# Kernel optimization log

Measured on AMD Instinct MI355X. Metric: run time of the kernel, lower is better.

Reference implementation:

```python
import jax, jax.numpy as jnp
import numpy as np

N = 100000
E = 1600000
IN_C = 128
HID = 256
K_EIG = 64
OUT_C = 16


def setup_inputs() -> dict:
    key = jax.random.key(0)
    ks = jax.random.split(key, 8)
    x = jax.random.normal(ks[0], (N, IN_C), dtype=jnp.float32)
    edge_index = jax.random.randint(ks[1], (2, E), 0, N)
    MLP_W = jax.random.normal(ks[2], (K_EIG, N), dtype=jnp.float32) * 0.02
    MLP_b = jax.random.normal(ks[3], (K_EIG,), dtype=jnp.float32) * 0.02
    mlpx_W = jax.random.normal(ks[4], (HID, IN_C), dtype=jnp.float32) * 0.05
    mlpx_b = jax.random.normal(ks[5], (HID,), dtype=jnp.float32) * 0.02
    fin_W = jax.random.normal(ks[6], (OUT_C, HID + K_EIG), dtype=jnp.float32) * 0.05
    fin_b = jax.random.normal(ks[7], (OUT_C,), dtype=jnp.float32) * 0.02
    return {"x": x, "edge_index": edge_index, "MLP_W": MLP_W, "MLP_b": MLP_b,
            "mlpx_W": mlpx_W, "mlpx_b": mlpx_b, "fin_W": fin_W, "fin_b": fin_b}


def _spmm(row, col, feats, n):
    # adj is COO with coords (col[e], row[e]) and value 1 -> out[col] += feats[row]
    return jax.ops.segment_sum(feats[row], col, num_segments=n)


def _pump(xA, row, col, n):
    # MinCut-style pump: soft assignment, normalized-cut loss + orthogonality loss
    S = jax.nn.softmax(xA, axis=-1)                      # [N, K]
    AS = _spmm(row, col, S, n)                            # A @ S, [N, K]
    cut = jnp.sum(S * AS)                                 # tr(S^T A S)
    deg = jax.ops.segment_sum(jnp.ones(col.shape, S.dtype), col, num_segments=n)
    deg_term = jnp.sum(deg[:, None] * S * S)              # tr(S^T D S)
    pump_loss = -(cut / deg_term)
    SS = S.T @ S                                          # [K, K]
    k = S.shape[1]
    ortho_loss = jnp.linalg.norm(SS / jnp.linalg.norm(SS)
                                 - jnp.eye(k, dtype=S.dtype) / jnp.sqrt(jnp.asarray(k, S.dtype)))
    return S, pump_loss, ortho_loss


def reference(x, edge_index, MLP_W, MLP_b, mlpx_W, mlpx_b, fin_W, fin_b):
    row, col = edge_index[0], edge_index[1]
    n = x.shape[0]
    # xA = adj @ MLP.weight.T + bias   (irregular gather/scatter over edges)
    xA = _spmm(row, col, MLP_W.T, n) + MLP_b              # [N, K]
    xX = x @ mlpx_W.T + mlpx_b                            # [N, HID]
    xA, pump_loss, ortho_loss = _pump(xA, row, col, n)
    z = jnp.concatenate([xX, xA], axis=1)                 # [N, HID+K]
    # dropout omitted (eval mode)
    z = jax.nn.log_softmax(z @ fin_W.T + fin_b, axis=-1)  # [N, OUT]
    return (z, pump_loss + ortho_loss)
```

## Files before the change

### kernel.cpp

```cpp
#include <hip/hip_runtime.h>
#include <math.h>

#define N_NODES 100000
#define N_EDGES 1600000
#define IN_C    128
#define HID     256
#define KEIG    64
#define OUT_C   16

#define NPB      256
#define NBUCKET  ((N_NODES + NPB - 1) / NPB)
#define EDGE_TILE 4096
#define NTILE    ((N_EDGES + EDGE_TILE - 1) / EDGE_TILE)
#define CAP      8960

#define TRANS_BLOCKS   ((N_NODES + 63) / 64)
#define GATHER_BLOCKS  2048
#define CUT_BLOCKS     2048
#define SSP_BLOCKS     512
#define OUTG_BLOCKS    384
#define TAIL_BLOCKS    (128 * 23)

typedef __attribute__((ext_vector_type(8))) short short8;
typedef __attribute__((ext_vector_type(4))) float f32x4;

__device__ __forceinline__ float wave_sum(float v) {
#pragma unroll
    for (int m = 32; m; m >>= 1) v += __shfl_xor(v, m, 64);
    return v;
}
__device__ __forceinline__ float wave_max(float v) {
#pragma unroll
    for (int m = 32; m; m >>= 1) v = fmaxf(v, __shfl_xor(v, m, 64));
    return v;
}
__device__ __forceinline__ float bf2f(unsigned int u) {
    return __uint_as_float((u & 0xffffu) << 16);
}
__device__ __forceinline__ unsigned short f2bf(float f) {
    unsigned int u = __float_as_uint(f);
    u += 0x7fff + ((u >> 16) & 1);
    return (unsigned short)(u >> 16);
}
__device__ __forceinline__ float fp8tof(int b) {
    return __builtin_amdgcn_cvt_f32_fp8(b, 0);
}
__device__ __forceinline__ unsigned char f2fp8(float f) {
    int p = __builtin_amdgcn_cvt_pk_fp8_f32(f, f, 0, false);
    return (unsigned char)(p & 0xff);
}

#define FMA4(P, s, W) \
    P.x = fmaf(s, W.x, P.x); P.y = fmaf(s, W.y, P.y); \
    P.z = fmaf(s, W.z, P.z); P.w = fmaf(s, W.w, P.w);

#define GATHER16(TBL, DST) do {                                               \
    int r0 = csr_row[ps + j + 0],  r1 = csr_row[ps + j + 1];                  \
    int r2 = csr_row[ps + j + 2],  r3 = csr_row[ps + j + 3];                  \
    int r4 = csr_row[ps + j + 4],  r5 = csr_row[ps + j + 5];                  \
    int r6 = csr_row[ps + j + 6],  r7 = csr_row[ps + j + 7];                  \
    int r8 = csr_row[ps + j + 8],  r9 = csr_row[ps + j + 9];                  \
    int rA = csr_row[ps + j + 10], rB = csr_row[ps + j + 11];                 \
    int rC = csr_row[ps + j + 12], rD = csr_row[ps + j + 13];                 \
    int rE = csr_row[ps + j + 14], rF = csr_row[ps + j + 15];                 \
    int b0 = TBL[(unsigned)r0 * 64u + lane], b1 = TBL[(unsigned)r1 * 64u + lane]; \
    int b2 = TBL[(unsigned)r2 * 64u + lane], b3 = TBL[(unsigned)r3 * 64u + lane]; \
    int b4 = TBL[(unsigned)r4 * 64u + lane], b5 = TBL[(unsigned)r5 * 64u + lane]; \
    int b6 = TBL[(unsigned)r6 * 64u + lane], b7 = TBL[(unsigned)r7 * 64u + lane]; \
    int b8 = TBL[(unsigned)r8 * 64u + lane], b9 = TBL[(unsigned)r9 * 64u + lane]; \
    int bA = TBL[(unsigned)rA * 64u + lane], bB = TBL[(unsigned)rB * 64u + lane]; \
    int bC = TBL[(unsigned)rC * 64u + lane], bD = TBL[(unsigned)rD * 64u + lane]; \
    int bE = TBL[(unsigned)rE * 64u + lane], bF = TBL[(unsigned)rF * 64u + lane]; \
    DST += (((fp8tof(b0) + fp8tof(b1)) + (fp8tof(b2) + fp8tof(b3)))           \
          + ((fp8tof(b4) + fp8tof(b5)) + (fp8tof(b6) + fp8tof(b7))))          \
         + (((fp8tof(b8) + fp8tof(b9)) + (fp8tof(bA) + fp8tof(bB)))           \
          + ((fp8tof(bC) + fp8tof(bD)) + (fp8tof(bE) + fp8tof(bF))));         \
} while (0)

__global__ void prep_weff(const float* __restrict__ mlpxW, const float* __restrict__ mlpxb,
                          const float* __restrict__ finW, const float* __restrict__ finb,
                          float* __restrict__ Weff, float* __restrict__ beff,
                          int* __restrict__ bcnt, unsigned char* __restrict__ WT8,
                          unsigned char* __restrict__ S8, int* __restrict__ gpad) {
    int t = blockIdx.x * blockDim.x + threadIdx.x;
    const int NW = (IN_C + KEIG) * OUT_C;
    if (t < NW) {
        int k = t >> 4, o = t & 15;
        float acc;
        if (k < IN_C) {
            acc = 0.f;
            for (int c = 0; c < HID; ++c)
                acc += mlpxW[c * IN_C + k] * finW[o * (HID + KEIG) + c];
        } else {
            acc = finW[o * (HID + KEIG) + HID + (k - IN_C)];
        }
        Weff[k * OUT_C + o] = acc;
    }
    int tb = t - NW;
    if (tb >= 0 && tb < OUT_C) {
        float acc = finb[tb];
        for (int c = 0; c < HID; ++c) acc += mlpxb[c] * finW[tb * (HID + KEIG) + c];
        beff[tb] = acc;
    }
    int tz = t - (NW + OUT_C);
    if (tz >= 0 && tz <= NBUCKET) bcnt[tz] = 0;
    int tp = t - (NW + OUT_C + NBUCKET + 1);
    if (tp >= 0 && tp < 16) {
        ((int*)(WT8 + (size_t)N_NODES * 64))[tp] = 0;
        ((int*)(S8 + (size_t)N_NODES * 64))[tp] = 0;
        if (tp == 0) *gpad = 0;
    }
}

__global__ __launch_bounds__(256) void fused_prep(const float* __restrict__ W,
                                                  unsigned char* __restrict__ WT8,
                                                  const int* __restrict__ ei,
                                                  int* __restrict__ bcnt) {
    __shared__ __align__(16) char sm[64 * 65 * 4];
    int t = threadIdx.x;
    if (blockIdx.x < TRANS_BLOCKS) {
        float (*tile)[65] = (float (*)[65])sm;
        int n0 = blockIdx.x * 64;
        int tn = t & 63, tq = t >> 6;
#pragma unroll
        for (int kk = 0; kk < 16; ++kk) {
            int k = tq * 16 + kk;
            int n = n0 + tn;
            tile[k][tn] = (n < N_NODES) ? W[(long long)k * N_NODES + n] : 0.f;
        }
        __syncthreads();
        int tk = t & 63;
#pragma unroll
        for (int ii = 0; ii < 16; ++ii) {
            int n = n0 + tq * 16 + ii;
            if (n < N_NODES) WT8[(unsigned)n * 64u + tk] = f2fp8(tile[tk][tq * 16 + ii] * 32.f);
        }
    } else {
        int* h = (int*)sm;
        for (int i = t; i < NBUCKET; i += 256) h[i] = 0;
        __syncthreads();
        int tile_i = blockIdx.x - TRANS_BLOCKS;
        int e0 = tile_i * EDGE_TILE;
        int e1 = min(e0 + EDGE_TILE, N_EDGES);
        for (int e = e0 + t; e < e1; e += 256)
            atomicAdd(&h[ei[N_EDGES + e] >> 8], 1);
        __syncthreads();
        for (int i = t; i < NBUCKET; i += 256)
            if (h[i]) atomicAdd(&bcnt[i], h[i]);
    }
}

__global__ void bucket_scan(const int* __restrict__ bcnt, int* __restrict__ bbase,
                            int* __restrict__ bcur) {
    __shared__ int sh[512];
    int t = threadIdx.x;
    int v = (t < NBUCKET) ? bcnt[t] : 0;
    sh[t] = v;
    __syncthreads();
    for (int d = 1; d < 512; d <<= 1) {
        int u = (t >= d) ? sh[t - d] : 0;
        __syncthreads();
        sh[t] += u;
        __syncthreads();
    }
    if (t < NBUCKET) { bbase[t] = sh[t] - v; bcur[t] = sh[t] - v; }
    if (t == 0) bbase[NBUCKET] = N_EDGES;
}

__global__ void bucket_scatter(const int* __restrict__ ei, int* __restrict__ bcur,
                               int* __restrict__ ebuf) {
    __shared__ int h[NBUCKET];
    __shared__ int gb[NBUCKET];
    __shared__ int lpre[NBUCKET];
    __shared__ int psum[256];
    __shared__ int stage[EDGE_TILE];
    __shared__ short bkt[EDGE_TILE];
    int t = threadIdx.x;
    for (int i = t; i < NBUCKET; i += 256) h[i] = 0;
    __syncthreads();
    int e0 = blockIdx.x * EDGE_TILE;
    int e1 = min(e0 + EDGE_TILE, N_EDGES);
    int nt = e1 - e0;
    for (int e = e0 + t; e < e1; e += 256)
        atomicAdd(&h[ei[N_EDGES + e] >> 8], 1);
    __syncthreads();
    int a0 = (2 * t < NBUCKET) ? h[2 * t] : 0;
    int a1 = (2 * t + 1 < NBUCKET) ? h[2 * t + 1] : 0;
    psum[t] = a0 + a1;
    __syncthreads();
    for (int d = 1; d < 256; d <<= 1) {
        int u = (t >= d) ? psum[t - d] : 0;
        __syncthreads();
        psum[t] += u;
        __syncthreads();
    }
    int base = (t == 0) ? 0 : psum[t - 1];
    if (2 * t < NBUCKET) lpre[2 * t] = base;
    if (2 * t + 1 < NBUCKET) lpre[2 * t + 1] = base + a0;
    __syncthreads();
    for (int i = t; i < NBUCKET; i += 256) {
        int c = h[i];
        gb[i] = c ? atomicAdd(&bcur[i], c) : 0;
        h[i] = lpre[i];
    }
    __syncthreads();
    for (int e = e0 + t; e < e1; e += 256) {
        int r = ei[e];
        int c = ei[N_EDGES + e];
        int b = c >> 8;
        int slot = atomicAdd(&h[b], 1);
        stage[slot] = r | ((c & 255) << 17);
        bkt[slot] = (short)b;
    }
    __syncthreads();
    for (int s = t; s < nt; s += 256) {
        int b = bkt[s];
        ebuf[gb[b] + s - lpre[b]] = stage[s];
    }
}

__global__ void csr_build(const int* __restrict__ ebuf, const int* __restrict__ bbase,
                          int* __restrict__ offsets, int* __restrict__ pstart,
                          int* __restrict__ csr_row, int* __restrict__ gpad) {
    __shared__ int hist[NPB];
    __shared__ int sh[NPB];
    __shared__ int curs[NPB];
    __shared__ int staged[CAP];
    __shared__ int pbase_sh;
    int b = blockIdx.x;
    int t = threadIdx.x;
    int s0 = bbase[b], s1 = bbase[b + 1];
    hist[t] = 0;
    __syncthreads();
    for (int i = s0 + t; i < s1; i += 256)
        atomicAdd(&hist[ebuf[i] >> 17], 1);
    __syncthreads();
    int v = hist[t];
    int pv = (v + 15) & ~15;
    sh[t] = pv;
    __syncthreads();
    for (int d = 1; d < 256; d <<= 1) {
        int u = (t >= d) ? sh[t - d] : 0;
        __syncthreads();
        sh[t] += u;
        __syncthreads();
    }
    int pexcl = sh[t] - pv;
    int pt = sh[255];
    if (t == 0) pbase_sh = atomicAdd(gpad, pt);
    __syncthreads();
    int pbase = pbase_sh;
    int node = b * NPB + t;
    if (node < N_NODES) { offsets[node] = v; pstart[node] = pbase + pexcl; }
    curs[t] = pexcl;
    __syncthreads();
    if (pt <= CAP) {
        for (int i = t; i < pt; i += 256) staged[i] = N_NODES;
        __syncthreads();
        for (int i = s0 + t; i < s1; i += 256) {
            int pk = ebuf[i];
            int pos = atomicAdd(&curs[pk >> 17], 1);
            staged[pos] = pk & 0x1FFFF;
        }
        __syncthreads();
        for (int i = t; i < pt; i += 256) csr_row[pbase + i] = staged[i];
    } else {
        for (int i = t; i < pt; i += 256) csr_row[pbase + i] = N_NODES;
        __syncthreads();
        for (int i = s0 + t; i < s1; i += 256) {
            int pk = ebuf[i];
            int pos = atomicAdd(&curs[pk >> 17], 1);
            csr_row[pbase + pos] = pk & 0x1FFFF;
        }
    }
}

__global__ void gather_softmax(const int* __restrict__ offsets, const int* __restrict__ pstart,
                               const int* __restrict__ csr_row,
                               const unsigned char* __restrict__ WT8,
                               const float* __restrict__ MLPb,
                               unsigned short* __restrict__ Sb,
                               unsigned char* __restrict__ S8,
                               float* __restrict__ dtp) {
    int lane = threadIdx.x & 63;
    int wib = __builtin_amdgcn_readfirstlane(threadIdx.x >> 6);
    int gw = blockIdx.x * 4 + wib;
    int nw = gridDim.x * 4;
    float bias = MLPb[lane];
    float dacc = 0.f;
    for (int n = gw; n < N_NODES; n += nw) {
        int deg = __builtin_amdgcn_readfirstlane(offsets[n]);
        int ps  = __builtin_amdgcn_readfirstlane(pstart[n]);
        int plen = (deg + 15) & ~15;
        float acc = 0.f;
        for (int j = 0; j < plen; j += 16) GATHER16(WT8, acc);
        acc = bias + acc * 0.03125f;
        float m = wave_max(acc);
        float e = __expf(acc - m);
        float sm = wave_sum(e);
        float sv = e / sm;
        unsigned idx = (unsigned)n * 64u + lane;
        Sb[idx] = f2bf(sv);
        S8[idx] = f2fp8(sv * 64.f);
        dacc += (float)deg * sv * sv;
    }
    dacc = wave_sum(dacc);
    __shared__ float red[4];
    if (lane == 0) red[wib] = dacc;
    __syncthreads();
    if (threadIdx.x == 0) dtp[blockIdx.x] = red[0] + red[1] + red[2] + red[3];
}

__global__ __launch_bounds__(256) void fused_tail(
        const int* __restrict__ offsets, const int* __restrict__ pstart,
        const int* __restrict__ csr_row,
        const unsigned short* __restrict__ Sb, const unsigned char* __restrict__ S8,
        float* __restrict__ cutp, float* __restrict__ ssp,
        const float* __restrict__ x, const float* __restrict__ Weff,
        const float* __restrict__ beff, float* __restrict__ out) {
    __shared__ __align__(16) char sm[768 * 16 + 64];
    int t = threadIdx.x;
    int grp = blockIdx.x / 23;
    int r23 = blockIdx.x % 23;

    if (r23 < 16) {
        int bid = grp * 16 + r23;
        int lane = t & 63;
        int wib = __builtin_amdgcn_readfirstlane(t >> 6);
        int gw = bid * 4 + wib;
        int nw = CUT_BLOCKS * 4;
        float acc = 0.f;
        for (int n = gw; n < N_NODES; n += nw) {
            float sc = bf2f(Sb[(unsigned)n * 64u + lane]);
            int deg = __builtin_amdgcn_readfirstlane(offsets[n]);
            int ps  = __builtin_amdgcn_readfirstlane(pstart[n]);
            int plen = (deg + 15) & ~15;
            float g = 0.f;
            for (int j = 0; j < plen; j += 16) GATHER16(S8, g);
            acc += sc * g * 0.015625f;
        }
        acc = wave_sum(acc);
        float* red = (float*)sm;
        if (lane == 0) red[wib] = acc;
        __syncthreads();
        if (t == 0) cutp[bid] = red[0] + red[1] + red[2] + red[3];
    } else if (r23 < 20) {
        int bid2 = grp * 4 + (r23 - 16);
        unsigned short (*Sr)[66] = (unsigned short (*)[66])sm;
        int lane = t & 63;
        int w = t >> 6;
        int m = lane & 15;
        int quad = lane >> 4;
        int srow = t >> 3;
        int spart = t & 7;
        f32x4 a0 = {0.f,0.f,0.f,0.f}, a1 = {0.f,0.f,0.f,0.f};
        f32x4 a2 = {0.f,0.f,0.f,0.f}, a3 = {0.f,0.f,0.f,0.f};
        for (int base = bid2 * 32; base < N_NODES; base += SSP_BLOCKS * 32) {
            const uint4* g = (const uint4*)(Sb + (long long)(base + srow) * 64 + spart * 8);
            uint4 d = *g;
            __syncthreads();
            unsigned int* rowp = (unsigned int*)&Sr[srow][0];
            rowp[spart * 4 + 0] = d.x;
            rowp[spart * 4 + 1] = d.y;
            rowp[spart * 4 + 2] = d.z;
            rowp[spart * 4 + 3] = d.w;
            __syncthreads();
            short8 f0, f1, f2, f3;
#pragma unroll
            for (int j = 0; j < 8; ++j) {
                int k = quad * 8 + j;
                f0[j] = (short)Sr[k][m];
                f1[j] = (short)Sr[k][16 + m];
                f2[j] = (short)Sr[k][32 + m];
                f3[j] = (short)Sr[k][48 + m];
            }
            short8 fa = (w == 0) ? f0 : (w == 1) ? f1 : (w == 2) ? f2 : f3;
            a0 = __builtin_amdgcn_mfma_f32_16x16x32_bf16(fa, f0, a0, 0, 0, 0);
            a1 = __builtin_amdgcn_mfma_f32_16x16x32_bf16(fa, f1, a1, 0, 0, 0);
            a2 = __builtin_amdgcn_mfma_f32_16x16x32_bf16(fa, f2, a2, 0, 0, 0);
            a3 = __builtin_amdgcn_mfma_f32_16x16x32_bf16(fa, f3, a3, 0, 0, 0);
        }
        float* dst = ssp + (size_t)bid2 * 4096;
#pragma unroll
        for (int r = 0; r < 4; ++r) {
            int row = w * 16 + quad * 4 + r;
            dst[row * 64 +  0 + m] = a0[r];
            dst[row * 64 + 16 + m] = a1[r];
            dst[row * 64 + 32 + m] = a2[r];
            dst[row * 64 + 48 + m] = a3[r];
        }
    } else {
        int obid = grp * 3 + (r23 - 20);
        float4* Wsh = (float4*)sm;
        float* bsh = (float*)(sm + 768 * 16);
        const float4* W4 = (const float4*)Weff;
        for (int i = t; i < 768; i += 256) Wsh[i] = W4[i];
        if (t < 16) bsh[t] = beff[t];
        __syncthreads();
        for (int r = obid * 256 + t; r < N_NODES; r += OUTG_BLOCKS * 256) {
            float4 p0 = make_float4(bsh[0], bsh[1], bsh[2], bsh[3]);
            float4 p1 = make_float4(bsh[4], bsh[5], bsh[6], bsh[7]);
            float4 p2 = make_float4(bsh[8], bsh[9], bsh[10], bsh[11]);
            float4 p3 = make_float4(bsh[12], bsh[13], bsh[14], bsh[15]);
            const float4* xr = (const float4*)(x + (long long)r * IN_C);
#pragma unroll 8
            for (int j = 0; j < 32; ++j) {
                float4 xv = xr[j];
                int k = j * 4;
                float xs[4] = {xv.x, xv.y, xv.z, xv.w};
#pragma unroll
                for (int c = 0; c < 4; ++c) {
                    float s = xs[c];
                    float4 w0 = Wsh[(k + c) * 4 + 0];
                    float4 w1 = Wsh[(k + c) * 4 + 1];
                    float4 w2 = Wsh[(k + c) * 4 + 2];
                    float4 w3 = Wsh[(k + c) * 4 + 3];
                    FMA4(p0, s, w0); FMA4(p1, s, w1); FMA4(p2, s, w2); FMA4(p3, s, w3);
                }
            }
            const uint2* sr = (const uint2*)(Sb + (long long)r * 64);
#pragma unroll 8
            for (int j = 0; j < 16; ++j) {
                uint2 u = sr[j];
                float xs[4] = {bf2f(u.x), bf2f(u.x >> 16), bf2f(u.y), bf2f(u.y >> 16)};
                int k = IN_C + j * 4;
#pragma unroll
                for (int c = 0; c < 4; ++c) {
                    float s = xs[c];
                    float4 w0 = Wsh[(k + c) * 4 + 0];
                    float4 w1 = Wsh[(k + c) * 4 + 1];
                    float4 w2 = Wsh[(k + c) * 4 + 2];
                    float4 w3 = Wsh[(k + c) * 4 + 3];
                    FMA4(p0, s, w0); FMA4(p1, s, w1); FMA4(p2, s, w2); FMA4(p3, s, w3);
                }
            }
            float m = fmaxf(fmaxf(fmaxf(p0.x, p0.y), fmaxf(p0.z, p0.w)),
                            fmaxf(fmaxf(fmaxf(p1.x, p1.y), fmaxf(p1.z, p1.w)),
                                  fmaxf(fmaxf(fmaxf(p2.x, p2.y), fmaxf(p2.z, p2.w)),
                                        fmaxf(fmaxf(p3.x, p3.y), fmaxf(p3.z, p3.w)))));
            float sum = __expf(p0.x - m) + __expf(p0.y - m) + __expf(p0.z - m) + __expf(p0.w - m)
                      + __expf(p1.x - m) + __expf(p1.y - m) + __expf(p1.z - m) + __expf(p1.w - m)
                      + __expf(p2.x - m) + __expf(p2.y - m) + __expf(p2.z - m) + __expf(p2.w - m)
                      + __expf(p3.x - m) + __expf(p3.y - m) + __expf(p3.z - m) + __expf(p3.w - m);
            float lse = m + logf(sum);
            float4* o4 = (float4*)(out + (long long)r * OUT_C);
            o4[0] = make_float4(p0.x - lse, p0.y - lse, p0.z - lse, p0.w - lse);
            o4[1] = make_float4(p1.x - lse, p1.y - lse, p1.z - lse, p1.w - lse);
            o4[2] = make_float4(p2.x - lse, p2.y - lse, p2.z - lse, p2.w - lse);
            o4[3] = make_float4(p3.x - lse, p3.y - lse, p3.z - lse, p3.w - lse);
        }
    }
}

__global__ void reduce_ss(const float* __restrict__ ssp, float* __restrict__ SS) {
    int e = blockIdx.x * blockDim.x + threadIdx.x;
    float s = 0.f;
    for (int p = 0; p < SSP_BLOCKS; ++p) s += ssp[(size_t)p * 4096 + e];
    SS[e] = s;
}

__global__ void scalars_kernel(const float* __restrict__ cutp, const float* __restrict__ dtp,
                               const float* __restrict__ SS, float* __restrict__ out) {
    __shared__ float red[256];
    int t = threadIdx.x;
    float c = 0.f;
    for (int i = t; i < CUT_BLOCKS; i += 256) c += cutp[i];
    red[t] = c; __syncthreads();
    for (int s = 128; s; s >>= 1) { if (t < s) red[t] += red[t + s]; __syncthreads(); }
    float cut = red[0]; __syncthreads();

    float d = 0.f;
    for (int i = t; i < GATHER_BLOCKS; i += 256) d += dtp[i];
    red[t] = d; __syncthreads();
    for (int s = 128; s; s >>= 1) { if (t < s) red[t] += red[t + s]; __syncthreads(); }
    float dterm = red[0]; __syncthreads();

    float ss[16];
    float sq = 0.f;
#pragma unroll
    for (int j = 0; j < 16; ++j) { ss[j] = SS[t * 16 + j]; sq += ss[j] * ss[j]; }
    red[t] = sq; __syncthreads();
    for (int s = 128; s; s >>= 1) { if (t < s) red[t] += red[t + s]; __syncthreads(); }
    float nrm = sqrtf(red[0]); __syncthreads();

    float osq = 0.f;
#pragma unroll
    for (int j = 0; j < 16; ++j) {
        int idx = t * 16 + j;
        float v = ss[j] / nrm - ((idx % 65 == 0) ? 0.125f : 0.f);
        osq += v * v;
    }
    red[t] = osq; __syncthreads();
    for (int s = 128; s; s >>= 1) { if (t < s) red[t] += red[t + s]; __syncthreads(); }
    if (t == 0) {
        float loss = -(cut / dterm) + sqrtf(red[0]);
        out[(long long)N_NODES * OUT_C] = loss;
    }
}

extern "C" void kernel_launch(void* const* d_in, const int* in_sizes, int n_in,
                              void* d_out, int out_size, void* d_ws, size_t ws_size,
                              hipStream_t stream) {
    const float* x     = (const float*)d_in[0];
    const int*   ei    = (const int*)d_in[1];
    const float* MLPW  = (const float*)d_in[2];
    const float* MLPb  = (const float*)d_in[3];
    const float* mlpxW = (const float*)d_in[4];
    const float* mlpxb = (const float*)d_in[5];
    const float* finW  = (const float*)d_in[6];
    const float* finb  = (const float*)d_in[7];
    float* out = (float*)d_out;
    char* ws = (char*)d_ws;

    unsigned char*  WT8 = (unsigned char*)ws;
    unsigned char*  S8  = (unsigned char*)(ws + (size_t)(N_NODES + 1) * 64);
    unsigned short* Sb  = (unsigned short*)(ws + (size_t)(N_NODES + 1) * 128);
    char* p = ws + (size_t)(N_NODES + 1) * 128 + (size_t)N_NODES * 128;
    float* ssp  = (float*)p;
    float* SS   = ssp + (size_t)SSP_BLOCKS * 4096;
    float* Weff = SS + 4096;
    float* beff = Weff + 192 * 16;
    float* cutp = beff + 16;
    float* dtp  = cutp + CUT_BLOCKS;
    int* ebuf    = (int*)(dtp + GATHER_BLOCKS);
    int* csr_row = ebuf + N_EDGES;
    int* offsets = csr_row + N_EDGES + 16 * N_NODES;
    int* pstart  = offsets + N_NODES + 1;
    int* bcnt    = pstart + N_NODES;
    int* bbase   = bcnt + NBUCKET + 1;
    int* bcur    = bbase + NBUCKET + 1;
    int* gpad    = bcur + NBUCKET;

    hipLaunchKernelGGL(prep_weff, dim3(16), dim3(256), 0, stream,
                       mlpxW, mlpxb, finW, finb, Weff, beff, bcnt, WT8, S8, gpad);
    hipLaunchKernelGGL(fused_prep, dim3(TRANS_BLOCKS + NTILE), dim3(256), 0, stream,
                       MLPW, WT8, ei, bcnt);
    hipLaunchKernelGGL(bucket_scan, dim3(1), dim3(512), 0, stream, bcnt, bbase, bcur);
    hipLaunchKernelGGL(bucket_scatter, dim3(NTILE), dim3(256), 0, stream, ei, bcur, ebuf);
    hipLaunchKernelGGL(csr_build, dim3(NBUCKET), dim3(256), 0, stream,
                       ebuf, bbase, offsets, pstart, csr_row, gpad);
    hipLaunchKernelGGL(gather_softmax, dim3(GATHER_BLOCKS), dim3(256), 0, stream,
                       offsets, pstart, csr_row, WT8, MLPb, Sb, S8, dtp);
    hipLaunchKernelGGL(fused_tail, dim3(TAIL_BLOCKS), dim3(256), 0, stream,
                       offsets, pstart, csr_row, Sb, S8, cutp, ssp, x, Weff, beff, out);
    hipLaunchKernelGGL(reduce_ss, dim3(16), dim3(256), 0, stream, ssp, SS);
    hipLaunchKernelGGL(scalars_kernel, dim3(1), dim3(256), 0, stream, cutp, dtp, SS, out);
}
```

Before: 305.5 us.

## Split wave into four edge lanes with packed fp8 row loads in gathers

The gather loops in gather_softmax and the cut part of fused_tail are restructured. Each wave now covers four edges at once: each 16-lane quarter handles one edge and loads 4 fp8 features per lane as one 32-bit word, replacing one byte per lane. Cross-quarter shuffles combine the partial sums, and the per-node softmax runs over 16 lanes with 4 values each. CSR padding drops from 16 to 4 so fewer padded dummy edges are gathered, and degree and start offset are packed into one int2 array. This costs extra shuffles and only a quarter of lanes do the stores, and the int4 loads of csr_row depend on 16-byte alignment that the padding to multiples of 4 keeps.

```diff
diff --git a/kernel.cpp b/kernel.cpp
--- a/kernel.cpp
+++ b/kernel.cpp
@@ -23,15 +23,11 @@
 
 typedef __attribute__((ext_vector_type(8))) short short8;
 typedef __attribute__((ext_vector_type(4))) float f32x4;
+typedef __attribute__((ext_vector_type(2))) float f32x2;
 
 __device__ __forceinline__ float wave_sum(float v) {
 #pragma unroll
     for (int m = 32; m; m >>= 1) v += __shfl_xor(v, m, 64);
-    return v;
-}
-__device__ __forceinline__ float wave_max(float v) {
-#pragma unroll
-    for (int m = 32; m; m >>= 1) v = fmaxf(v, __shfl_xor(v, m, 64));
     return v;
 }
 __device__ __forceinline__ float bf2f(unsigned int u) {
@@ -42,9 +38,6 @@
     u += 0x7fff + ((u >> 16) & 1);
     return (unsigned short)(u >> 16);
 }
-__device__ __forceinline__ float fp8tof(int b) {
-    return __builtin_amdgcn_cvt_f32_fp8(b, 0);
-}
 __device__ __forceinline__ unsigned char f2fp8(float f) {
     int p = __builtin_amdgcn_cvt_pk_fp8_f32(f, f, 0, false);
     return (unsigned char)(p & 0xff);
@@ -54,27 +47,36 @@
     P.x = fmaf(s, W.x, P.x); P.y = fmaf(s, W.y, P.y); \
     P.z = fmaf(s, W.z, P.z); P.w = fmaf(s, W.w, P.w);
 
-#define GATHER16(TBL, DST) do {                                               \
-    int r0 = csr_row[ps + j + 0],  r1 = csr_row[ps + j + 1];                  \
-    int r2 = csr_row[ps + j + 2],  r3 = csr_row[ps + j + 3];                  \
-    int r4 = csr_row[ps + j + 4],  r5 = csr_row[ps + j + 5];                  \
-    int r6 = csr_row[ps + j + 6],  r7 = csr_row[ps + j + 7];                  \
-    int r8 = csr_row[ps + j + 8],  r9 = csr_row[ps + j + 9];                  \
-    int rA = csr_row[ps + j + 10], rB = csr_row[ps + j + 11];                 \
-    int rC = csr_row[ps + j + 12], rD = csr_row[ps + j + 13];                 \
-    int rE = csr_row[ps + j + 14], rF = csr_row[ps + j + 15];                 \
-    int b0 = TBL[(unsigned)r0 * 64u + lane], b1 = TBL[(unsigned)r1 * 64u + lane]; \
-    int b2 = TBL[(unsigned)r2 * 64u + lane], b3 = TBL[(unsigned)r3 * 64u + lane]; \
-    int b4 = TBL[(unsigned)r4 * 64u + lane], b5 = TBL[(unsigned)r5 * 64u + lane]; \
-    int b6 = TBL[(unsigned)r6 * 64u + lane], b7 = TBL[(unsigned)r7 * 64u + lane]; \
-    int b8 = TBL[(unsigned)r8 * 64u + lane], b9 = TBL[(unsigned)r9 * 64u + lane]; \
-    int bA = TBL[(unsigned)rA * 64u + lane], bB = TBL[(unsigned)rB * 64u + lane]; \
-    int bC = TBL[(unsigned)rC * 64u + lane], bD = TBL[(unsigned)rD * 64u + lane]; \
-    int bE = TBL[(unsigned)rE * 64u + lane], bF = TBL[(unsigned)rF * 64u + lane]; \
-    DST += (((fp8tof(b0) + fp8tof(b1)) + (fp8tof(b2) + fp8tof(b3)))           \
-          + ((fp8tof(b4) + fp8tof(b5)) + (fp8tof(b6) + fp8tof(b7))))          \
-         + (((fp8tof(b8) + fp8tof(b9)) + (fp8tof(bA) + fp8tof(bB)))           \
-          + ((fp8tof(bC) + fp8tof(bD)) + (fp8tof(bE) + fp8tof(bF))));         \
+#define GSEL(RR) (q == 0 ? RR.x : q == 1 ? RR.y : q == 2 ? RR.z : RR.w)
+
+#define GATHER4V(TBL, DST) do {                                                  \
+    int4 ra_ = *(const int4*)(csr_row + ps + j);                                 \
+    int r0_ = GSEL(ra_);                                                         \
+    unsigned u0_ = *(const unsigned*)(TBL + (unsigned)r0_ * 64u + cb);           \
+    f32x2 p_;                                                                    \
+    p_ = __builtin_amdgcn_cvt_pk_f32_fp8(u0_, false); DST.x += p_.x; DST.y += p_.y; \
+    p_ = __builtin_amdgcn_cvt_pk_f32_fp8(u0_, true);  DST.z += p_.x; DST.w += p_.y; \
+} while (0)
+
+#define GATHER16V(TBL, DST) do {                                                 \
+    int4 ra_ = *(const int4*)(csr_row + ps + j);                                 \
+    int4 rb_ = *(const int4*)(csr_row + ps + j + 4);                             \
+    int4 rc_ = *(const int4*)(csr_row + ps + j + 8);                             \
+    int4 rd_ = *(const int4*)(csr_row + ps + j + 12);                            \
+    int r0_ = GSEL(ra_), r1_ = GSEL(rb_), r2_ = GSEL(rc_), r3_ = GSEL(rd_);      \
+    unsigned u0_ = *(const unsigned*)(TBL + (unsigned)r0_ * 64u + cb);           \
+    unsigned u1_ = *(const unsigned*)(TBL + (unsigned)r1_ * 64u + cb);           \
+    unsigned u2_ = *(const unsigned*)(TBL + (unsigned)r2_ * 64u + cb);           \
+    unsigned u3_ = *(const unsigned*)(TBL + (unsigned)r3_ * 64u + cb);           \
+    f32x2 p_;                                                                    \
+    p_ = __builtin_amdgcn_cvt_pk_f32_fp8(u0_, false); DST.x += p_.x; DST.y += p_.y; \
+    p_ = __builtin_amdgcn_cvt_pk_f32_fp8(u0_, true);  DST.z += p_.x; DST.w += p_.y; \
+    p_ = __builtin_amdgcn_cvt_pk_f32_fp8(u1_, false); DST.x += p_.x; DST.y += p_.y; \
+    p_ = __builtin_amdgcn_cvt_pk_f32_fp8(u1_, true);  DST.z += p_.x; DST.w += p_.y; \
+    p_ = __builtin_amdgcn_cvt_pk_f32_fp8(u2_, false); DST.x += p_.x; DST.y += p_.y; \
+    p_ = __builtin_amdgcn_cvt_pk_f32_fp8(u2_, true);  DST.z += p_.x; DST.w += p_.y; \
+    p_ = __builtin_amdgcn_cvt_pk_f32_fp8(u3_, false); DST.x += p_.x; DST.y += p_.y; \
+    p_ = __builtin_amdgcn_cvt_pk_f32_fp8(u3_, true);  DST.z += p_.x; DST.w += p_.y; \
 } while (0)
 
 __global__ void prep_weff(const float* __restrict__ mlpxW, const float* __restrict__ mlpxb,
@@ -220,7 +222,7 @@
 }
 
 __global__ void csr_build(const int* __restrict__ ebuf, const int* __restrict__ bbase,
-                          int* __restrict__ offsets, int* __restrict__ pstart,
+                          int2* __restrict__ nodei,
                           int* __restrict__ csr_row, int* __restrict__ gpad) {
     __shared__ int hist[NPB];
     __shared__ int sh[NPB];
@@ -236,7 +238,7 @@
         atomicAdd(&hist[ebuf[i] >> 17], 1);
     __syncthreads();
     int v = hist[t];
-    int pv = (v + 15) & ~15;
+    int pv = (v + 3) & ~3;
     sh[t] = pv;
     __syncthreads();
     for (int d = 1; d < 256; d <<= 1) {
@@ -251,7 +253,7 @@
     __syncthreads();
     int pbase = pbase_sh;
     int node = b * NPB + t;
-    if (node < N_NODES) { offsets[node] = v; pstart[node] = pbase + pexcl; }
+    if (node < N_NODES) nodei[node] = make_int2(v, pbase + pexcl);
     curs[t] = pexcl;
     __syncthreads();
     if (pt <= CAP) {
@@ -275,7 +277,7 @@
     }
 }
 
-__global__ void gather_softmax(const int* __restrict__ offsets, const int* __restrict__ pstart,
+__global__ void gather_softmax(const int2* __restrict__ nodei,
                                const int* __restrict__ csr_row,
                                const unsigned char* __restrict__ WT8,
                                const float* __restrict__ MLPb,
@@ -283,36 +285,62 @@
                                unsigned char* __restrict__ S8,
                                float* __restrict__ dtp) {
     int lane = threadIdx.x & 63;
+    int q = lane >> 4;
+    unsigned cb = (unsigned)(lane & 15) * 4u;
     int wib = __builtin_amdgcn_readfirstlane(threadIdx.x >> 6);
     int gw = blockIdx.x * 4 + wib;
     int nw = gridDim.x * 4;
-    float bias = MLPb[lane];
+    f32x4 bias = *(const f32x4*)(MLPb + (lane & 15) * 4);
     float dacc = 0.f;
     for (int n = gw; n < N_NODES; n += nw) {
-        int deg = __builtin_amdgcn_readfirstlane(offsets[n]);
-        int ps  = __builtin_amdgcn_readfirstlane(pstart[n]);
-        int plen = (deg + 15) & ~15;
-        float acc = 0.f;
-        for (int j = 0; j < plen; j += 16) GATHER16(WT8, acc);
-        acc = bias + acc * 0.03125f;
-        float m = wave_max(acc);
-        float e = __expf(acc - m);
-        float sm = wave_sum(e);
-        float sv = e / sm;
-        unsigned idx = (unsigned)n * 64u + lane;
-        Sb[idx] = f2bf(sv);
-        S8[idx] = f2fp8(sv * 64.f);
-        dacc += (float)deg * sv * sv;
+        int2 di = nodei[n];
+        int deg = __builtin_amdgcn_readfirstlane(di.x);
+        int ps  = __builtin_amdgcn_readfirstlane(di.y);
+        int plen = (deg + 3) & ~3;
+        f32x4 acc = {0.f, 0.f, 0.f, 0.f};
+        int j = 0;
+        for (; j + 16 <= plen; j += 16) { GATHER16V(WT8, acc); }
+        for (; j < plen; j += 4) { GATHER4V(WT8, acc); }
+#pragma unroll
+        for (int mm = 16; mm < 64; mm <<= 1) {
+            acc.x += __shfl_xor(acc.x, mm, 64);
+            acc.y += __shfl_xor(acc.y, mm, 64);
+            acc.z += __shfl_xor(acc.z, mm, 64);
+            acc.w += __shfl_xor(acc.w, mm, 64);
+        }
+        float ax = bias.x + acc.x * 0.03125f;
+        float ay = bias.y + acc.y * 0.03125f;
+        float az = bias.z + acc.z * 0.03125f;
+        float aw = bias.w + acc.w * 0.03125f;
+        float m4 = fmaxf(fmaxf(ax, ay), fmaxf(az, aw));
+#pragma unroll
+        for (int mm = 1; mm < 16; mm <<= 1) m4 = fmaxf(m4, __shfl_xor(m4, mm, 64));
+        float ex = __expf(ax - m4), ey = __expf(ay - m4);
+        float ez = __expf(az - m4), ew = __expf(aw - m4);
+        float s4 = (ex + ey) + (ez + ew);
+#pragma unroll
+        for (int mm = 1; mm < 16; mm <<= 1) s4 += __shfl_xor(s4, mm, 64);
+        float inv = 1.f / s4;
+        float sx = ex * inv, sy = ey * inv, sz = ez * inv, sw = ew * inv;
+        if (q == 0) {
+            unsigned lo = (unsigned)f2bf(sx) | ((unsigned)f2bf(sy) << 16);
+            unsigned hi = (unsigned)f2bf(sz) | ((unsigned)f2bf(sw) << 16);
+            *(uint2*)(Sb + (unsigned)n * 64u + cb) = make_uint2(lo, hi);
+            int p8 = __builtin_amdgcn_cvt_pk_fp8_f32(sx * 64.f, sy * 64.f, 0, false);
+            p8 = __builtin_amdgcn_cvt_pk_fp8_f32(sz * 64.f, sw * 64.f, p8, true);
+            *(unsigned*)(S8 + (unsigned)n * 64u + cb) = (unsigned)p8;
+        }
+        dacc += (float)deg * ((sx * sx + sy * sy) + (sz * sz + sw * sw));
     }
     dacc = wave_sum(dacc);
     __shared__ float red[4];
-    if (lane == 0) red[wib] = dacc;
+    if (lane == 0) red[wib] = dacc * 0.25f;
     __syncthreads();
     if (threadIdx.x == 0) dtp[blockIdx.x] = red[0] + red[1] + red[2] + red[3];
 }
 
 __global__ __launch_bounds__(256) void fused_tail(
-        const int* __restrict__ offsets, const int* __restrict__ pstart,
+        const int2* __restrict__ nodei,
         const int* __restrict__ csr_row,
         const unsigned short* __restrict__ Sb, const unsigned char* __restrict__ S8,
         float* __restrict__ cutp, float* __restrict__ ssp,
@@ -326,22 +354,28 @@
     if (r23 < 16) {
         int bid = grp * 16 + r23;
         int lane = t & 63;
+        int q = lane >> 4;
+        unsigned cb = (unsigned)(lane & 15) * 4u;
         int wib = __builtin_amdgcn_readfirstlane(t >> 6);
         int gw = bid * 4 + wib;
         int nw = CUT_BLOCKS * 4;
         float acc = 0.f;
         for (int n = gw; n < N_NODES; n += nw) {
-            float sc = bf2f(Sb[(unsigned)n * 64u + lane]);
-            int deg = __builtin_amdgcn_readfirstlane(offsets[n]);
-            int ps  = __builtin_amdgcn_readfirstlane(pstart[n]);
-            int plen = (deg + 15) & ~15;
-            float g = 0.f;
-            for (int j = 0; j < plen; j += 16) GATHER16(S8, g);
-            acc += sc * g * 0.015625f;
+            int2 di = nodei[n];
+            int deg = __builtin_amdgcn_readfirstlane(di.x);
+            int ps  = __builtin_amdgcn_readfirstlane(di.y);
+            uint2 su = *(const uint2*)(Sb + (unsigned)n * 64u + cb);
+            int plen = (deg + 3) & ~3;
+            f32x4 g = {0.f, 0.f, 0.f, 0.f};
+            int j = 0;
+            for (; j + 16 <= plen; j += 16) { GATHER16V(S8, g); }
+            for (; j < plen; j += 4) { GATHER4V(S8, g); }
+            acc += bf2f(su.x) * g.x + bf2f(su.x >> 16) * g.y
+                 + bf2f(su.y) * g.z + bf2f(su.y >> 16) * g.w;
         }
         acc = wave_sum(acc);
         float* red = (float*)sm;
-        if (lane == 0) red[wib] = acc;
+        if (lane == 0) red[wib] = acc * 0.015625f;
         __syncthreads();
         if (t == 0) cutp[bid] = red[0] + red[1] + red[2] + red[3];
     } else if (r23 < 20) {
@@ -524,9 +558,8 @@
     float* dtp  = cutp + CUT_BLOCKS;
     int* ebuf    = (int*)(dtp + GATHER_BLOCKS);
     int* csr_row = ebuf + N_EDGES;
-    int* offsets = csr_row + N_EDGES + 16 * N_NODES;
-    int* pstart  = offsets + N_NODES + 1;
-    int* bcnt    = pstart + N_NODES;
+    int2* nodei  = (int2*)(csr_row + N_EDGES + 16 * N_NODES);
+    int* bcnt    = (int*)(nodei + N_NODES);
     int* bbase   = bcnt + NBUCKET + 1;
     int* bcur    = bbase + NBUCKET + 1;
     int* gpad    = bcur + NBUCKET;
@@ -538,11 +571,11 @@
     hipLaunchKernelGGL(bucket_scan, dim3(1), dim3(512), 0, stream, bcnt, bbase, bcur);
     hipLaunchKernelGGL(bucket_scatter, dim3(NTILE), dim3(256), 0, stream, ei, bcur, ebuf);
     hipLaunchKernelGGL(csr_build, dim3(NBUCKET), dim3(256), 0, stream,
-                       ebuf, bbase, offsets, pstart, csr_row, gpad);
+                       ebuf, bbase, nodei, csr_row, gpad);
     hipLaunchKernelGGL(gather_softmax, dim3(GATHER_BLOCKS), dim3(256), 0, stream,
-                       offsets, pstart, csr_row, WT8, MLPb, Sb, S8, dtp);
+                       nodei, csr_row, WT8, MLPb, Sb, S8, dtp);
     hipLaunchKernelGGL(fused_tail, dim3(TAIL_BLOCKS), dim3(256), 0, stream,
-                       offsets, pstart, csr_row, Sb, S8, cutp, ssp, x, Weff, beff, out);
+                       nodei, csr_row, Sb, S8, cutp, ssp, x, Weff, beff, out);
     hipLaunchKernelGGL(reduce_ss, dim3(16), dim3(256), 0, stream, ssp, SS);
     hipLaunchKernelGGL(scalars_kernel, dim3(1), dim3(256), 0, stream, cutp, dtp, SS, out);
 }
```

After: 305.2 us. Within noise of the previous version (-0.1%).
